# Performance work log

Hardware: AMD Instinct MI355X
Metric: run time of the kernel (lower is better)

The kernel has to match this reference:

```python
import jax, jax.numpy as jnp
import numpy as np

N_USERS = 4096
N_ITEMS = 4096
D = 64
L = 2
B = 4096
N = N_USERS + N_ITEMS


def setup_inputs() -> dict:
    key = jax.random.key(0)
    ks = jax.random.split(key, 24)
    g = lambda i, shape: jax.random.normal(ks[i], shape, dtype=jnp.float32) * 0.05
    # sparse-ish 0/1 adjacency (module calls adj.to_dense(); ~16 neighbors/node)
    adj = (jax.random.uniform(ks[0], (N, N), dtype=jnp.float32) < 0.002).astype(jnp.float32)
    users = jax.random.randint(ks[1], (B,), 0, N_USERS)
    pos_items = jax.random.randint(ks[2], (B,), 0, N_ITEMS)
    neg_items = jax.random.randint(ks[3], (B,), 0, N_ITEMS)
    return {
        "adj_matrix": adj,
        "users": users,
        "pos_items": pos_items,
        "neg_items": neg_items,
        "user_table": g(4, (N_USERS, D)),
        "item_table": g(5, (N_ITEMS, D)),
        "gcn_W": g(6, (L, D, D)), "gcn_b": g(7, (L, D)),
        "gat_W": g(8, (L, D, D)), "gat_b": g(9, (L, D)),
        "attn_W": g(10, (L, 2 * D)), "attn_b": g(11, (L,)),
        "fuse_W": g(12, (L, 2 * D, D)), "fuse_b": g(13, (L, D)),
        "actor_W": g(14, (D, D)), "actor_b": g(15, (D,)),
        "critic_W1": g(16, (2 * D, D)), "critic_b1": g(17, (D,)),
        "critic_W2": g(18, (D, 1)), "critic_b2": g(19, (1,)),
        "layer_weights": jnp.ones((L,), dtype=jnp.float32),
    }


def _leaky(x):
    return jnp.where(x >= 0, x, 0.01 * x)  # F.leaky_relu default slope


def reference(adj_matrix, users, pos_items, neg_items, user_table, item_table,
              gcn_W, gcn_b, gat_W, gat_b, attn_W, attn_b, fuse_W, fuse_b,
              actor_W, actor_b, critic_W1, critic_b1, critic_W2, critic_b2,
              layer_weights):
    all_emb = jnp.concatenate([user_table, item_table], axis=0)  # [N, D]

    # GCN stack: spmm(adj, x) then linear, relu
    gcn = [all_emb]
    for l in range(L):
        h = adj_matrix @ gcn[-1]
        gcn.append(jax.nn.relu(h @ gcn_W[l] + gcn_b[l]))

    # GAT stack: e[i,j] = leaky_relu(a1.h_i + a2.h_j + b); multiply-mask by adj, row softmax
    gat = [all_emb]
    for l in range(L):
        h = gat[-1] @ gat_W[l] + gat_b[l]  # [N, D]
        a1, a2 = attn_W[l, :D], attn_W[l, D:]
        e = _leaky((h @ a1)[:, None] + (h @ a2)[None, :] + attn_b[l])  # [N, N]
        attn = jax.nn.softmax(e * adj_matrix, axis=1)  # faithful: multiply-mask, not -inf
        gat.append(jax.nn.relu(attn @ h))

    lw = jax.nn.softmax(layer_weights)
    fused = jnp.zeros((N, D), dtype=all_emb.dtype)
    for i in range(L):
        cat = jnp.concatenate([gcn[i + 1], gat[i + 1]], axis=1)  # [N, 2D]
        fused = fused + lw[i] * jax.nn.relu(cat @ fuse_W[i] + fuse_b[i])

    user_emb, item_emb = fused[:N_USERS], fused[N_USERS:]
    u = user_emb[users]
    p = item_emb[pos_items]
    n = item_emb[neg_items]

    uf = u @ actor_W + actor_b  # Actor
    pos_score = jnp.sum(uf * p, axis=1)
    neg_score = jnp.sum(uf * n, axis=1)

    def critic(a, b):
        x = jnp.concatenate([a, b], axis=1)
        hidden = jax.nn.relu(x @ critic_W1 + critic_b1)
        return hidden @ critic_W2 + critic_b2

    return pos_score, neg_score, critic(u, p), critic(u, n)
```

## Files before the change

kernel.cpp:

```cpp
#include <hip/hip_runtime.h>

#define NTOT 8192
#define NROW 2048
#define NU 4096
#define D 64
#define MAXN 64
#define ND (NTOT*D)

__device__ __forceinline__ float wsum(float x){
  #pragma unroll
  for(int o=32;o;o>>=1) x += __shfl_xor(x,o);
  return x;
}
__device__ __forceinline__ float wmax(float x){
  #pragma unroll
  for(int o=32;o;o>>=1) x = fmaxf(x,__shfl_xor(x,o));
  return x;
}
__device__ __forceinline__ float bcastf(float x, int k){
  return __uint_as_float(__builtin_amdgcn_readlane(__float_as_uint(x), (unsigned)k));
}
__device__ __forceinline__ int bcasti(int x, int k){
  return (int)__builtin_amdgcn_readlane((unsigned)x, (unsigned)k);
}

__device__ __forceinline__ float gat_attn_row(const float* __restrict__ h,
    const float* __restrict__ kvv, const float* __restrict__ S,
    const int* __restrict__ cols, int cnt, float q, float ab, int lane){
  int t = lane;
  int col = (t < cnt) ? cols[t] : 0;
  float e = -1e30f;
  if(t < cnt){
    float xx = q + kvv[col] + ab;
    e = (xx >= 0.f) ? xx : 0.01f * xx;
  }
  float m  = fmaxf(0.f, wmax(e));
  float w  = (t < cnt) ? expf(e - m) : 0.f;
  float em = expf(-m);
  float Z  = (float)(NTOT - cnt) * em + wsum(w);
  float acc = 0.f, hsum = 0.f;
  for(int tt = 0; tt < cnt; ++tt){
    float wt = bcastf(w, tt);
    int   jc = bcasti(col, tt);
    float hv = h[jc*D + lane];
    acc  = fmaf(wt, hv, acc);
    hsum += hv;
  }
  float outv = (acc + em * (S[lane] - hsum)) / Z;
  return fmaxf(outv, 0.f);
}

__global__ __launch_bounds__(256) void kA(const float* __restrict__ adj,
    const float* __restrict__ ut, const float* __restrict__ it,
    float* __restrict__ all_emb, int* __restrict__ ell, int* __restrict__ nnz,
    float* __restrict__ Svec0, float* __restrict__ Svec1, float* __restrict__ gcn1){
  int bid = blockIdx.x, tid = threadIdx.x;
  if(bid < NROW){
    int lane = tid & 63;
    int row  = bid*4 + (tid >> 6);
    ell[row*MAXN + lane] = NTOT;
    const float4* arow = (const float4*)(adj + (size_t)row * NTOT);
    int base = 0;
    for(int c0 = 0; c0 < NTOT/4; c0 += 64){
      float4 v = arow[c0 + lane];
      int nib = (v.x!=0.f?1:0) | (v.y!=0.f?2:0) | (v.z!=0.f?4:0) | (v.w!=0.f?8:0);
      if(__ballot(nib != 0) == 0ull) continue;
      #pragma unroll
      for(int j = 0; j < 4; ++j){
        unsigned long long m = __ballot(((nib>>j)&1) != 0);
        if(m){
          if((nib>>j)&1){
            int below = __builtin_amdgcn_mbcnt_hi((unsigned)(m>>32),
                        __builtin_amdgcn_mbcnt_lo((unsigned)m, 0u));
            int slot = base + below;
            if(slot < MAXN) ell[row*MAXN + slot] = (c0 + lane)*4 + j;
          }
          base += __popcll(m);
        }
      }
    }
    if(lane == 0) nnz[row] = base > MAXN ? MAXN : base;
  } else if(bid < 2*NROW){
    int i = (bid - NROW)*256 + tid;
    all_emb[i] = (i < NU*D) ? ut[i] : it[i - NU*D];
  } else {
    if(tid < D){
      Svec0[tid] = 0.f; Svec1[tid] = 0.f;
      all_emb[ND + tid] = 0.f;
      gcn1[ND + tid]    = 0.f;
    }
  }
}

__global__ __launch_bounds__(256) void kB(const float* __restrict__ all_emb,
    const int* __restrict__ ell, const int* __restrict__ nnz,
    const float* __restrict__ gcn_W, const float* __restrict__ gcn_b,
    const float* __restrict__ gat_W, const float* __restrict__ gat_b,
    const float* __restrict__ attn_W,
    float* __restrict__ gcn1, float* __restrict__ h0,
    float* __restrict__ qv0, float* __restrict__ kv0, float* __restrict__ Svec0){
  __shared__ float Ws[D*D];
  __shared__ float red[4][D];
  int tid = threadIdx.x, lane = tid & 63, wid = tid >> 6;
  int bid = blockIdx.x;
  if(bid < NROW){
    for(int i = tid; i < D*D; i += 256) Ws[i] = gcn_W[i];
    __syncthreads();
    int row = bid*4 + wid;
    int cnt = nnz[row];
    const int* cols = ell + row*MAXN;
    float acc = 0.f;
    int cnt8 = (cnt + 7) & ~7;
    for(int t = 0; t < cnt8; t += 8){
      #pragma unroll
      for(int u = 0; u < 8; ++u){
        int j = cols[t + u];
        acc += all_emb[j*D + lane];
      }
    }
    float y = gcn_b[lane];
    #pragma unroll 16
    for(int k = 0; k < D; ++k) y = fmaf(bcastf(acc, k), Ws[k*D + lane], y);
    gcn1[row*D + lane] = fmaxf(y, 0.f);
  } else {
    for(int i = tid; i < D*D; i += 256) Ws[i] = gat_W[i];
    __syncthreads();
    int row = (bid - NROW)*4 + wid;
    float xr = all_emb[row*D + lane];
    float h = gat_b[lane];
    #pragma unroll 16
    for(int k = 0; k < D; ++k) h = fmaf(bcastf(xr, k), Ws[k*D + lane], h);
    h0[row*D + lane] = h;
    float q  = wsum(h * attn_W[lane]);
    float kk = wsum(h * attn_W[D + lane]);
    if(lane == 0){ qv0[row] = q; kv0[row] = kk; }
    red[wid][lane] = h;
    __syncthreads();
    if(wid == 0){
      float s = red[0][lane] + red[1][lane] + red[2][lane] + red[3][lane];
      atomicAdd(&Svec0[lane], s);
    }
  }
}

__global__ __launch_bounds__(256) void kC(
    const float* __restrict__ all_emb, const int* __restrict__ ell, const int* __restrict__ nnz,
    const float* __restrict__ gcn1, const float* __restrict__ h0,
    const float* __restrict__ qv0, const float* __restrict__ kv0, const float* __restrict__ Svec0,
    const float* __restrict__ gcn_W, const float* __restrict__ gcn_b,
    const float* __restrict__ gat_W, const float* __restrict__ gat_b,
    const float* __restrict__ attn_W, const float* __restrict__ attn_b,
    const float* __restrict__ fuse_W, const float* __restrict__ fuse_b,
    const float* __restrict__ layer_w,
    float* __restrict__ gcn2, float* __restrict__ h1,
    float* __restrict__ qv1, float* __restrict__ kv1, float* __restrict__ Svec1,
    float* __restrict__ fusedb){
  __shared__ float Ws[D*D];
  __shared__ float red[4][D];
  int tid = threadIdx.x, lane = tid & 63, wid = tid >> 6;
  int bid = blockIdx.x;
  if(bid < NROW){
    for(int i = tid; i < D*D; i += 256) Ws[i] = gcn_W[D*D + i];
    __syncthreads();
    int row = bid*4 + wid;
    int cnt = nnz[row];
    const int* cols = ell + row*MAXN;
    float acc = 0.f;
    int cnt8 = (cnt + 7) & ~7;
    for(int t = 0; t < cnt8; t += 8){
      #pragma unroll
      for(int u = 0; u < 8; ++u){
        int j = cols[t + u];
        acc += gcn1[j*D + lane];
      }
    }
    float y = gcn_b[D + lane];
    #pragma unroll 16
    for(int k = 0; k < D; ++k) y = fmaf(bcastf(acc, k), Ws[k*D + lane], y);
    gcn2[row*D + lane] = fmaxf(y, 0.f);
  } else {
    int row = (bid - NROW)*4 + wid;
    int cnt = nnz[row];
    const int* cols = ell + row*MAXN;
    float g1 = gat_attn_row(h0, kv0, Svec0, cols, cnt, qv0[row], attn_b[0], lane);
    float gc1 = gcn1[row*D + lane];
    float l0 = layer_w[0], l1 = layer_w[1];
    float mx = fmaxf(l0, l1);
    float e0 = expf(l0 - mx), e1 = expf(l1 - mx);
    float lw0 = e0 / (e0 + e1);
    for(int i = tid; i < D*D; i += 256) Ws[i] = fuse_W[i];
    __syncthreads();
    float y = fuse_b[lane];
    #pragma unroll 16
    for(int k = 0; k < D; ++k) y = fmaf(bcastf(gc1, k), Ws[k*D + lane], y);
    __syncthreads();
    for(int i = tid; i < D*D; i += 256) Ws[i] = fuse_W[D*D + i];
    __syncthreads();
    #pragma unroll 16
    for(int k = 0; k < D; ++k) y = fmaf(bcastf(g1, k), Ws[k*D + lane], y);
    fusedb[row*D + lane] = lw0 * fmaxf(y, 0.f);
    __syncthreads();
    for(int i = tid; i < D*D; i += 256) Ws[i] = gat_W[D*D + i];
    __syncthreads();
    float h = gat_b[D + lane];
    #pragma unroll 16
    for(int k = 0; k < D; ++k) h = fmaf(bcastf(g1, k), Ws[k*D + lane], h);
    h1[row*D + lane] = h;
    float qq = wsum(h * attn_W[2*D + lane]);
    float kk = wsum(h * attn_W[3*D + lane]);
    if(lane == 0){ qv1[row] = qq; kv1[row] = kk; }
    red[wid][lane] = h;
    __syncthreads();
    if(wid == 0){
      float s = red[0][lane] + red[1][lane] + red[2][lane] + red[3][lane];
      atomicAdd(&Svec1[lane], s);
    }
  }
}

__global__ __launch_bounds__(256) void kE(
    const int* __restrict__ ell, const int* __restrict__ nnz,
    const float* __restrict__ gcn2, const float* __restrict__ h1,
    const float* __restrict__ qv1, const float* __restrict__ kv1, const float* __restrict__ Svec1,
    const float* __restrict__ attn_b,
    const float* __restrict__ fuse_W, const float* __restrict__ fuse_b,
    const float* __restrict__ layer_w,
    float* __restrict__ fusedb){
  __shared__ float Ws[D*D];
  int tid = threadIdx.x, lane = tid & 63, wid = tid >> 6;
  int row = blockIdx.x*4 + wid;
  int cnt = nnz[row];
  const int* cols = ell + row*MAXN;
  float g2 = gat_attn_row(h1, kv1, Svec1, cols, cnt, qv1[row], attn_b[1], lane);
  float gc2 = gcn2[row*D + lane];
  float l0 = layer_w[0], l1 = layer_w[1];
  float mx = fmaxf(l0, l1);
  float e0 = expf(l0 - mx), e1 = expf(l1 - mx);
  float lw1 = e1 / (e0 + e1);
  for(int i = tid; i < D*D; i += 256) Ws[i] = fuse_W[2*D*D + i];
  __syncthreads();
  float y = fuse_b[D + lane];
  #pragma unroll 16
  for(int k = 0; k < D; ++k) y = fmaf(bcastf(gc2, k), Ws[k*D + lane], y);
  __syncthreads();
  for(int i = tid; i < D*D; i += 256) Ws[i] = fuse_W[3*D*D + i];
  __syncthreads();
  #pragma unroll 16
  for(int k = 0; k < D; ++k) y = fmaf(bcastf(g2, k), Ws[k*D + lane], y);
  fusedb[row*D + lane] += lw1 * fmaxf(y, 0.f);
}

__global__ __launch_bounds__(256) void kF(const float* __restrict__ fused,
    const int* __restrict__ users, const int* __restrict__ pos, const int* __restrict__ neg,
    const float* __restrict__ AW, const float* __restrict__ abias,
    const float* __restrict__ cW1, const float* __restrict__ cb1,
    const float* __restrict__ cW2, const float* __restrict__ cb2,
    float* __restrict__ out){
  __shared__ float AWs[D*D];
  __shared__ float C1s[2*D*D];
  __shared__ float abs_[D], cb1s[D], C2s[D];
  int tid = threadIdx.x;
  for(int i = tid; i < D*D; i += 256) AWs[i] = AW[i];
  for(int i = tid; i < 2*D*D; i += 256) C1s[i] = cW1[i];
  if(tid < D){
    abs_[tid] = abias[tid];
    cb1s[tid] = cb1[tid];
    C2s[tid]  = cW2[tid];
  }
  __syncthreads();
  int lane = tid & 63;
  int bi   = blockIdx.x*4 + (tid >> 6);
  int ui = users[bi], pi = pos[bi] + NU, ni = neg[bi] + NU;
  float ud = fused[ui*D + lane], pd = fused[pi*D + lane], nd = fused[ni*D + lane];
  float ufd = abs_[lane];
  #pragma unroll 16
  for(int k = 0; k < D; ++k) ufd = fmaf(bcastf(ud, k), AWs[k*D + lane], ufd);
  float ps = wsum(ufd * pd);
  float ns = wsum(ufd * nd);
  float hu = cb1s[lane];
  #pragma unroll 16
  for(int k = 0; k < D; ++k) hu = fmaf(bcastf(ud, k), C1s[k*D + lane], hu);
  float hp = hu, hn = hu;
  #pragma unroll 16
  for(int k = 0; k < D; ++k){
    float pk = bcastf(pd, k), nk = bcastf(nd, k);
    hp = fmaf(pk, C1s[(D+k)*D + lane], hp);
    hn = fmaf(nk, C1s[(D+k)*D + lane], hn);
  }
  hp = fmaxf(hp, 0.f); hn = fmaxf(hn, 0.f);
  float cp = wsum(hp * C2s[lane]);
  float cn = wsum(hn * C2s[lane]);
  if(lane == 0){
    out[bi]         = ps;
    out[4096  + bi] = ns;
    out[8192  + bi] = cp + cb2[0];
    out[12288 + bi] = cn + cb2[0];
  }
}

extern "C" void kernel_launch(void* const* d_in, const int* in_sizes, int n_in,
                              void* d_out, int out_size, void* d_ws, size_t ws_size,
                              hipStream_t stream){
  const float* adj        = (const float*)d_in[0];
  const int*   users      = (const int*)d_in[1];
  const int*   pos        = (const int*)d_in[2];
  const int*   neg        = (const int*)d_in[3];
  const float* user_table = (const float*)d_in[4];
  const float* item_table = (const float*)d_in[5];
  const float* gcn_W      = (const float*)d_in[6];
  const float* gcn_b      = (const float*)d_in[7];
  const float* gat_W      = (const float*)d_in[8];
  const float* gat_b      = (const float*)d_in[9];
  const float* attn_W     = (const float*)d_in[10];
  const float* attn_b     = (const float*)d_in[11];
  const float* fuse_W     = (const float*)d_in[12];
  const float* fuse_b     = (const float*)d_in[13];
  const float* actor_W    = (const float*)d_in[14];
  const float* actor_b    = (const float*)d_in[15];
  const float* cW1        = (const float*)d_in[16];
  const float* cb1        = (const float*)d_in[17];
  const float* cW2        = (const float*)d_in[18];
  const float* cb2        = (const float*)d_in[19];
  const float* layer_w    = (const float*)d_in[20];

  float* ws      = (float*)d_ws;
  float* all_emb = ws;
  float* gcn1    = all_emb + ND + D;
  float* gcn2    = gcn1 + ND + D;
  float* h0      = gcn2 + ND;
  float* h1      = h0 + ND;
  float* fusedb  = h1 + ND;
  float* qv0     = fusedb + ND;
  float* kv0     = qv0 + NTOT;
  float* qv1     = kv0 + NTOT;
  float* kv1     = qv1 + NTOT;
  float* Svec0   = kv1 + NTOT;
  float* Svec1   = Svec0 + D;
  int*   nnz     = (int*)(Svec1 + D);
  int*   ell     = nnz + NTOT;

  kA<<<2*NROW + 1, 256, 0, stream>>>(adj, user_table, item_table,
                                     all_emb, ell, nnz, Svec0, Svec1, gcn1);
  kB<<<2*NROW, 256, 0, stream>>>(all_emb, ell, nnz, gcn_W, gcn_b, gat_W, gat_b,
                                 attn_W, gcn1, h0, qv0, kv0, Svec0);
  kC<<<2*NROW, 256, 0, stream>>>(all_emb, ell, nnz, gcn1, h0, qv0, kv0, Svec0,
                                 gcn_W, gcn_b, gat_W, gat_b, attn_W, attn_b,
                                 fuse_W, fuse_b, layer_w,
                                 gcn2, h1, qv1, kv1, Svec1, fusedb);
  kE<<<NROW, 256, 0, stream>>>(ell, nnz, gcn2, h1, qv1, kv1, Svec1, attn_b,
                               fuse_W, fuse_b, layer_w, fusedb);
  kF<<<1024, 256, 0, stream>>>(fusedb, users, pos, neg, actor_W, actor_b,
                               cW1, cb1, cW2, cb2, (float*)d_out);
}
```

Baseline: 221.1 us.

## Fuse adjacency scan with layer-1 GCN/GAT and replace atomics with partial-sum reduction

Restructures the pipeline: the GAT layer-0 projection runs first, then one kernel scans the dense adjacency row into a shared-memory column list and immediately performs GCN and GAT layer-1 aggregation, fusion and the next projection. Layer-2 GCN aggregation moves into the final per-row kernel, so GCN and GAT gathers share one neighbour loop. Atomic column sums are replaced by per-block partials reduced in a small single-block kernel, and adjacency loads are marked nontemporal. This cuts the number of passes and launches over the data, at the cost of two tiny serial reduction launches and heavier per-block work.

```diff
diff --git a/kernel.cpp b/kernel.cpp
--- a/kernel.cpp
+++ b/kernel.cpp
@@ -7,6 +7,8 @@
 #define MAXN 64
 #define ND (NTOT*D)
 
+typedef float f4 __attribute__((ext_vector_type(4)));
+
 __device__ __forceinline__ float wsum(float x){
   #pragma unroll
   for(int o=32;o;o>>=1) x += __shfl_xor(x,o);
@@ -18,210 +20,160 @@
   return x;
 }
 __device__ __forceinline__ float bcastf(float x, int k){
-  return __uint_as_float(__builtin_amdgcn_readlane(__float_as_uint(x), (unsigned)k));
+  return __uint_as_float(__builtin_amdgcn_readlane(__float_as_uint(x),(unsigned)k));
 }
 __device__ __forceinline__ int bcasti(int x, int k){
-  return (int)__builtin_amdgcn_readlane((unsigned)x, (unsigned)k);
-}
-
-__device__ __forceinline__ float gat_attn_row(const float* __restrict__ h,
-    const float* __restrict__ kvv, const float* __restrict__ S,
-    const int* __restrict__ cols, int cnt, float q, float ab, int lane){
-  int t = lane;
-  int col = (t < cnt) ? cols[t] : 0;
-  float e = -1e30f;
-  if(t < cnt){
-    float xx = q + kvv[col] + ab;
-    e = (xx >= 0.f) ? xx : 0.01f * xx;
-  }
-  float m  = fmaxf(0.f, wmax(e));
-  float w  = (t < cnt) ? expf(e - m) : 0.f;
-  float em = expf(-m);
-  float Z  = (float)(NTOT - cnt) * em + wsum(w);
-  float acc = 0.f, hsum = 0.f;
-  for(int tt = 0; tt < cnt; ++tt){
-    float wt = bcastf(w, tt);
-    int   jc = bcasti(col, tt);
-    float hv = h[jc*D + lane];
-    acc  = fmaf(wt, hv, acc);
-    hsum += hv;
-  }
-  float outv = (acc + em * (S[lane] - hsum)) / Z;
-  return fmaxf(outv, 0.f);
-}
-
-__global__ __launch_bounds__(256) void kA(const float* __restrict__ adj,
-    const float* __restrict__ ut, const float* __restrict__ it,
-    float* __restrict__ all_emb, int* __restrict__ ell, int* __restrict__ nnz,
-    float* __restrict__ Svec0, float* __restrict__ Svec1, float* __restrict__ gcn1){
-  int bid = blockIdx.x, tid = threadIdx.x;
-  if(bid < NROW){
-    int lane = tid & 63;
-    int row  = bid*4 + (tid >> 6);
-    ell[row*MAXN + lane] = NTOT;
-    const float4* arow = (const float4*)(adj + (size_t)row * NTOT);
-    int base = 0;
-    for(int c0 = 0; c0 < NTOT/4; c0 += 64){
-      float4 v = arow[c0 + lane];
-      int nib = (v.x!=0.f?1:0) | (v.y!=0.f?2:0) | (v.z!=0.f?4:0) | (v.w!=0.f?8:0);
-      if(__ballot(nib != 0) == 0ull) continue;
-      #pragma unroll
-      for(int j = 0; j < 4; ++j){
-        unsigned long long m = __ballot(((nib>>j)&1) != 0);
-        if(m){
-          if((nib>>j)&1){
-            int below = __builtin_amdgcn_mbcnt_hi((unsigned)(m>>32),
-                        __builtin_amdgcn_mbcnt_lo((unsigned)m, 0u));
-            int slot = base + below;
-            if(slot < MAXN) ell[row*MAXN + slot] = (c0 + lane)*4 + j;
-          }
-          base += __popcll(m);
-        }
-      }
-    }
-    if(lane == 0) nnz[row] = base > MAXN ? MAXN : base;
-  } else if(bid < 2*NROW){
-    int i = (bid - NROW)*256 + tid;
-    all_emb[i] = (i < NU*D) ? ut[i] : it[i - NU*D];
-  } else {
-    if(tid < D){
-      Svec0[tid] = 0.f; Svec1[tid] = 0.f;
-      all_emb[ND + tid] = 0.f;
-      gcn1[ND + tid]    = 0.f;
-    }
-  }
-}
-
-__global__ __launch_bounds__(256) void kB(const float* __restrict__ all_emb,
-    const int* __restrict__ ell, const int* __restrict__ nnz,
-    const float* __restrict__ gcn_W, const float* __restrict__ gcn_b,
-    const float* __restrict__ gat_W, const float* __restrict__ gat_b,
-    const float* __restrict__ attn_W,
-    float* __restrict__ gcn1, float* __restrict__ h0,
-    float* __restrict__ qv0, float* __restrict__ kv0, float* __restrict__ Svec0){
+  return (int)__builtin_amdgcn_readlane((unsigned)x,(unsigned)k);
+}
+
+__global__ __launch_bounds__(256) void k0a(const float* __restrict__ ut, const float* __restrict__ it,
+    const float* __restrict__ gat_W, const float* __restrict__ gat_b, const float* __restrict__ attn_W,
+    float* __restrict__ all_emb, float* __restrict__ h0,
+    float* __restrict__ q0v, float* __restrict__ k0v, float* __restrict__ part0){
   __shared__ float Ws[D*D];
   __shared__ float red[4][D];
   int tid = threadIdx.x, lane = tid & 63, wid = tid >> 6;
-  int bid = blockIdx.x;
-  if(bid < NROW){
-    for(int i = tid; i < D*D; i += 256) Ws[i] = gcn_W[i];
-    __syncthreads();
-    int row = bid*4 + wid;
-    int cnt = nnz[row];
-    const int* cols = ell + row*MAXN;
-    float acc = 0.f;
-    int cnt8 = (cnt + 7) & ~7;
-    for(int t = 0; t < cnt8; t += 8){
-      #pragma unroll
-      for(int u = 0; u < 8; ++u){
-        int j = cols[t + u];
-        acc += all_emb[j*D + lane];
-      }
-    }
-    float y = gcn_b[lane];
-    #pragma unroll 16
-    for(int k = 0; k < D; ++k) y = fmaf(bcastf(acc, k), Ws[k*D + lane], y);
-    gcn1[row*D + lane] = fmaxf(y, 0.f);
-  } else {
-    for(int i = tid; i < D*D; i += 256) Ws[i] = gat_W[i];
-    __syncthreads();
-    int row = (bid - NROW)*4 + wid;
-    float xr = all_emb[row*D + lane];
-    float h = gat_b[lane];
-    #pragma unroll 16
-    for(int k = 0; k < D; ++k) h = fmaf(bcastf(xr, k), Ws[k*D + lane], h);
-    h0[row*D + lane] = h;
-    float q  = wsum(h * attn_W[lane]);
-    float kk = wsum(h * attn_W[D + lane]);
-    if(lane == 0){ qv0[row] = q; kv0[row] = kk; }
-    red[wid][lane] = h;
-    __syncthreads();
-    if(wid == 0){
-      float s = red[0][lane] + red[1][lane] + red[2][lane] + red[3][lane];
-      atomicAdd(&Svec0[lane], s);
-    }
-  }
-}
-
-__global__ __launch_bounds__(256) void kC(
-    const float* __restrict__ all_emb, const int* __restrict__ ell, const int* __restrict__ nnz,
-    const float* __restrict__ gcn1, const float* __restrict__ h0,
-    const float* __restrict__ qv0, const float* __restrict__ kv0, const float* __restrict__ Svec0,
+  for(int i = tid; i < D*D; i += 256) Ws[i] = gat_W[i];
+  __syncthreads();
+  int row = blockIdx.x*4 + wid;
+  float x = (row < NU) ? ut[row*D + lane] : it[(row-NU)*D + lane];
+  all_emb[row*D + lane] = x;
+  float h = gat_b[lane];
+  #pragma unroll 16
+  for(int k = 0; k < D; ++k) h = fmaf(bcastf(x, k), Ws[k*D + lane], h);
+  h0[row*D + lane] = h;
+  float q  = wsum(h * attn_W[lane]);
+  float kk = wsum(h * attn_W[D + lane]);
+  if(lane == 0){ q0v[row] = q; k0v[row] = kk; }
+  red[wid][lane] = h;
+  __syncthreads();
+  if(wid == 0)
+    part0[blockIdx.x*D + lane] = red[0][lane] + red[1][lane] + red[2][lane] + red[3][lane];
+}
+
+__global__ __launch_bounds__(256) void kred(const float* __restrict__ part, float* __restrict__ S){
+  __shared__ float red[4][D];
+  int tid = threadIdx.x, lane = tid & 63, w = tid >> 6;
+  float s = 0.f;
+  for(int i = w; i < NROW; i += 4) s += part[i*D + lane];
+  red[w][lane] = s;
+  __syncthreads();
+  if(tid < D) S[tid] = red[0][tid] + red[1][tid] + red[2][tid] + red[3][tid];
+}
+
+__global__ __launch_bounds__(256) void k1(const float* __restrict__ adj,
+    const float* __restrict__ all_emb, const float* __restrict__ h0,
+    const float* __restrict__ q0v, const float* __restrict__ k0v, const float* __restrict__ S0,
     const float* __restrict__ gcn_W, const float* __restrict__ gcn_b,
     const float* __restrict__ gat_W, const float* __restrict__ gat_b,
     const float* __restrict__ attn_W, const float* __restrict__ attn_b,
     const float* __restrict__ fuse_W, const float* __restrict__ fuse_b,
     const float* __restrict__ layer_w,
-    float* __restrict__ gcn2, float* __restrict__ h1,
-    float* __restrict__ qv1, float* __restrict__ kv1, float* __restrict__ Svec1,
-    float* __restrict__ fusedb){
+    int* __restrict__ ell, int* __restrict__ nnz,
+    float* __restrict__ gcn1, float* __restrict__ fusedb, float* __restrict__ h1,
+    float* __restrict__ q1v, float* __restrict__ k1v, float* __restrict__ part1){
   __shared__ float Ws[D*D];
+  __shared__ int colbuf[4][MAXN];
   __shared__ float red[4][D];
   int tid = threadIdx.x, lane = tid & 63, wid = tid >> 6;
-  int bid = blockIdx.x;
-  if(bid < NROW){
-    for(int i = tid; i < D*D; i += 256) Ws[i] = gcn_W[D*D + i];
-    __syncthreads();
-    int row = bid*4 + wid;
-    int cnt = nnz[row];
-    const int* cols = ell + row*MAXN;
-    float acc = 0.f;
-    int cnt8 = (cnt + 7) & ~7;
-    for(int t = 0; t < cnt8; t += 8){
-      #pragma unroll
-      for(int u = 0; u < 8; ++u){
-        int j = cols[t + u];
-        acc += gcn1[j*D + lane];
+  int row = blockIdx.x*4 + wid;
+
+  const f4* arow = (const f4*)(adj + (size_t)row * NTOT);
+  int base = 0;
+  for(int c0 = 0; c0 < NTOT/4; c0 += 64){
+    f4 v = __builtin_nontemporal_load(&arow[c0 + lane]);
+    int nib = (v.x!=0.f?1:0) | (v.y!=0.f?2:0) | (v.z!=0.f?4:0) | (v.w!=0.f?8:0);
+    if(__ballot(nib != 0) == 0ull) continue;
+    #pragma unroll
+    for(int j = 0; j < 4; ++j){
+      unsigned long long m = __ballot(((nib>>j)&1) != 0);
+      if(m){
+        if((nib>>j)&1){
+          int below = __builtin_amdgcn_mbcnt_hi((unsigned)(m>>32),
+                      __builtin_amdgcn_mbcnt_lo((unsigned)m, 0u));
+          int slot = base + below;
+          if(slot < MAXN) colbuf[wid][slot] = (c0 + lane)*4 + j;
+        }
+        base += __popcll(m);
       }
     }
-    float y = gcn_b[D + lane];
-    #pragma unroll 16
-    for(int k = 0; k < D; ++k) y = fmaf(bcastf(acc, k), Ws[k*D + lane], y);
-    gcn2[row*D + lane] = fmaxf(y, 0.f);
-  } else {
-    int row = (bid - NROW)*4 + wid;
-    int cnt = nnz[row];
-    const int* cols = ell + row*MAXN;
-    float g1 = gat_attn_row(h0, kv0, Svec0, cols, cnt, qv0[row], attn_b[0], lane);
-    float gc1 = gcn1[row*D + lane];
-    float l0 = layer_w[0], l1 = layer_w[1];
-    float mx = fmaxf(l0, l1);
-    float e0 = expf(l0 - mx), e1 = expf(l1 - mx);
-    float lw0 = e0 / (e0 + e1);
-    for(int i = tid; i < D*D; i += 256) Ws[i] = fuse_W[i];
-    __syncthreads();
-    float y = fuse_b[lane];
-    #pragma unroll 16
-    for(int k = 0; k < D; ++k) y = fmaf(bcastf(gc1, k), Ws[k*D + lane], y);
-    __syncthreads();
-    for(int i = tid; i < D*D; i += 256) Ws[i] = fuse_W[D*D + i];
-    __syncthreads();
-    #pragma unroll 16
-    for(int k = 0; k < D; ++k) y = fmaf(bcastf(g1, k), Ws[k*D + lane], y);
-    fusedb[row*D + lane] = lw0 * fmaxf(y, 0.f);
-    __syncthreads();
-    for(int i = tid; i < D*D; i += 256) Ws[i] = gat_W[D*D + i];
-    __syncthreads();
-    float h = gat_b[D + lane];
-    #pragma unroll 16
-    for(int k = 0; k < D; ++k) h = fmaf(bcastf(g1, k), Ws[k*D + lane], h);
-    h1[row*D + lane] = h;
-    float qq = wsum(h * attn_W[2*D + lane]);
-    float kk = wsum(h * attn_W[3*D + lane]);
-    if(lane == 0){ qv1[row] = qq; kv1[row] = kk; }
-    red[wid][lane] = h;
-    __syncthreads();
-    if(wid == 0){
-      float s = red[0][lane] + red[1][lane] + red[2][lane] + red[3][lane];
-      atomicAdd(&Svec1[lane], s);
-    }
-  }
-}
-
-__global__ __launch_bounds__(256) void kE(
+  }
+  int cnt = base > MAXN ? MAXN : base;
+  int mycol = colbuf[wid][lane];
+  if(lane == 0) nnz[row] = cnt;
+  ell[row*MAXN + lane] = mycol;
+
+  float q  = q0v[row];
+  float ab = attn_b[0];
+  int colg = (lane < cnt) ? mycol : 0;
+  float e = -1e30f;
+  if(lane < cnt){
+    float xx = q + k0v[colg] + ab;
+    e = (xx >= 0.f) ? xx : 0.01f * xx;
+  }
+  float m  = fmaxf(0.f, wmax(e));
+  float w  = (lane < cnt) ? expf(e - m) : 0.f;
+  float em = expf(-m);
+  float Z  = (float)(NTOT - cnt) * em + wsum(w);
+
+  float accg = 0.f, acca = 0.f, hs = 0.f;
+  for(int tt = 0; tt < cnt; ++tt){
+    int   c  = bcasti(mycol, tt);
+    float wt = bcastf(w, tt);
+    float ev = all_emb[c*D + lane];
+    float hv = h0[c*D + lane];
+    accg += ev;
+    acca  = fmaf(wt, hv, acca);
+    hs   += hv;
+  }
+  float g1 = fmaxf((acca + em*(S0[lane] - hs)) / Z, 0.f);
+
+  for(int i = tid; i < D*D; i += 256) Ws[i] = gcn_W[i];
+  __syncthreads();
+  float yg = gcn_b[lane];
+  #pragma unroll 16
+  for(int k = 0; k < D; ++k) yg = fmaf(bcastf(accg, k), Ws[k*D + lane], yg);
+  float gc1 = fmaxf(yg, 0.f);
+  gcn1[row*D + lane] = gc1;
+  __syncthreads();
+
+  float l0 = layer_w[0], l1 = layer_w[1];
+  float mx = fmaxf(l0, l1);
+  float e0 = expf(l0 - mx), e1 = expf(l1 - mx);
+  float lw0 = e0 / (e0 + e1);
+  for(int i = tid; i < D*D; i += 256) Ws[i] = fuse_W[i];
+  __syncthreads();
+  float y = fuse_b[lane];
+  #pragma unroll 16
+  for(int k = 0; k < D; ++k) y = fmaf(bcastf(gc1, k), Ws[k*D + lane], y);
+  __syncthreads();
+  for(int i = tid; i < D*D; i += 256) Ws[i] = fuse_W[D*D + i];
+  __syncthreads();
+  #pragma unroll 16
+  for(int k = 0; k < D; ++k) y = fmaf(bcastf(g1, k), Ws[k*D + lane], y);
+  fusedb[row*D + lane] = lw0 * fmaxf(y, 0.f);
+  __syncthreads();
+
+  for(int i = tid; i < D*D; i += 256) Ws[i] = gat_W[D*D + i];
+  __syncthreads();
+  float h = gat_b[D + lane];
+  #pragma unroll 16
+  for(int k = 0; k < D; ++k) h = fmaf(bcastf(g1, k), Ws[k*D + lane], h);
+  h1[row*D + lane] = h;
+  float qq = wsum(h * attn_W[2*D + lane]);
+  float kk = wsum(h * attn_W[3*D + lane]);
+  if(lane == 0){ q1v[row] = qq; k1v[row] = kk; }
+  red[wid][lane] = h;
+  __syncthreads();
+  if(wid == 0)
+    part1[blockIdx.x*D + lane] = red[0][lane] + red[1][lane] + red[2][lane] + red[3][lane];
+}
+
+__global__ __launch_bounds__(256) void k2(
     const int* __restrict__ ell, const int* __restrict__ nnz,
-    const float* __restrict__ gcn2, const float* __restrict__ h1,
-    const float* __restrict__ qv1, const float* __restrict__ kv1, const float* __restrict__ Svec1,
+    const float* __restrict__ gcn1, const float* __restrict__ h1,
+    const float* __restrict__ q1v, const float* __restrict__ k1v, const float* __restrict__ S1,
+    const float* __restrict__ gcn_W, const float* __restrict__ gcn_b,
     const float* __restrict__ attn_b,
     const float* __restrict__ fuse_W, const float* __restrict__ fuse_b,
     const float* __restrict__ layer_w,
@@ -230,9 +182,39 @@
   int tid = threadIdx.x, lane = tid & 63, wid = tid >> 6;
   int row = blockIdx.x*4 + wid;
   int cnt = nnz[row];
-  const int* cols = ell + row*MAXN;
-  float g2 = gat_attn_row(h1, kv1, Svec1, cols, cnt, qv1[row], attn_b[1], lane);
-  float gc2 = gcn2[row*D + lane];
+  int mycol = ell[row*MAXN + lane];
+  float q  = q1v[row];
+  float ab = attn_b[1];
+  int colg = (lane < cnt) ? mycol : 0;
+  float e = -1e30f;
+  if(lane < cnt){
+    float xx = q + k1v[colg] + ab;
+    e = (xx >= 0.f) ? xx : 0.01f * xx;
+  }
+  float m  = fmaxf(0.f, wmax(e));
+  float w  = (lane < cnt) ? expf(e - m) : 0.f;
+  float em = expf(-m);
+  float Z  = (float)(NTOT - cnt) * em + wsum(w);
+  float accg = 0.f, acca = 0.f, hs = 0.f;
+  for(int tt = 0; tt < cnt; ++tt){
+    int   c  = bcasti(mycol, tt);
+    float wt = bcastf(w, tt);
+    float gv = gcn1[c*D + lane];
+    float hv = h1[c*D + lane];
+    accg += gv;
+    acca  = fmaf(wt, hv, acca);
+    hs   += hv;
+  }
+  float g2 = fmaxf((acca + em*(S1[lane] - hs)) / Z, 0.f);
+
+  for(int i = tid; i < D*D; i += 256) Ws[i] = gcn_W[D*D + i];
+  __syncthreads();
+  float yg = gcn_b[D + lane];
+  #pragma unroll 16
+  for(int k = 0; k < D; ++k) yg = fmaf(bcastf(accg, k), Ws[k*D + lane], yg);
+  float gc2 = fmaxf(yg, 0.f);
+  __syncthreads();
+
   float l0 = layer_w[0], l1 = layer_w[1];
   float mx = fmaxf(l0, l1);
   float e0 = expf(l0 - mx), e1 = expf(l1 - mx);
@@ -250,7 +232,7 @@
   fusedb[row*D + lane] += lw1 * fmaxf(y, 0.f);
 }
 
-__global__ __launch_bounds__(256) void kF(const float* __restrict__ fused,
+__global__ __launch_bounds__(256) void k3(const float* __restrict__ fused,
     const int* __restrict__ users, const int* __restrict__ pos, const int* __restrict__ neg,
     const float* __restrict__ AW, const float* __restrict__ abias,
     const float* __restrict__ cW1, const float* __restrict__ cb1,
@@ -325,30 +307,32 @@
 
   float* ws      = (float*)d_ws;
   float* all_emb = ws;
-  float* gcn1    = all_emb + ND + D;
-  float* gcn2    = gcn1 + ND + D;
-  float* h0      = gcn2 + ND;
+  float* h0      = all_emb + ND;
   float* h1      = h0 + ND;
-  float* fusedb  = h1 + ND;
-  float* qv0     = fusedb + ND;
-  float* kv0     = qv0 + NTOT;
-  float* qv1     = kv0 + NTOT;
-  float* kv1     = qv1 + NTOT;
-  float* Svec0   = kv1 + NTOT;
-  float* Svec1   = Svec0 + D;
-  int*   nnz     = (int*)(Svec1 + D);
+  float* gcn1    = h1 + ND;
+  float* fusedb  = gcn1 + ND;
+  float* q0v     = fusedb + ND;
+  float* k0v     = q0v + NTOT;
+  float* q1v     = k0v + NTOT;
+  float* k1v     = q1v + NTOT;
+  float* S0      = k1v + NTOT;
+  float* S1      = S0 + D;
+  float* part0   = S1 + D;
+  float* part1   = part0 + NROW*D;
+  int*   nnz     = (int*)(part1 + NROW*D);
   int*   ell     = nnz + NTOT;
 
-  kA<<<2*NROW + 1, 256, 0, stream>>>(adj, user_table, item_table,
-                                     all_emb, ell, nnz, Svec0, Svec1, gcn1);
-  kB<<<2*NROW, 256, 0, stream>>>(all_emb, ell, nnz, gcn_W, gcn_b, gat_W, gat_b,
-                                 attn_W, gcn1, h0, qv0, kv0, Svec0);
-  kC<<<2*NROW, 256, 0, stream>>>(all_emb, ell, nnz, gcn1, h0, qv0, kv0, Svec0,
-                                 gcn_W, gcn_b, gat_W, gat_b, attn_W, attn_b,
-                                 fuse_W, fuse_b, layer_w,
-                                 gcn2, h1, qv1, kv1, Svec1, fusedb);
-  kE<<<NROW, 256, 0, stream>>>(ell, nnz, gcn2, h1, qv1, kv1, Svec1, attn_b,
-                               fuse_W, fuse_b, layer_w, fusedb);
-  kF<<<1024, 256, 0, stream>>>(fusedb, users, pos, neg, actor_W, actor_b,
+  k0a<<<NROW, 256, 0, stream>>>(user_table, item_table, gat_W, gat_b, attn_W,
+                                all_emb, h0, q0v, k0v, part0);
+  kred<<<1, 256, 0, stream>>>(part0, S0);
+  k1<<<NROW, 256, 0, stream>>>(adj, all_emb, h0, q0v, k0v, S0,
+                               gcn_W, gcn_b, gat_W, gat_b, attn_W, attn_b,
+                               fuse_W, fuse_b, layer_w,
+                               ell, nnz, gcn1, fusedb, h1, q1v, k1v, part1);
+  kred<<<1, 256, 0, stream>>>(part1, S1);
+  k2<<<NROW, 256, 0, stream>>>(ell, nnz, gcn1, h1, q1v, k1v, S1,
+                               gcn_W, gcn_b, attn_b, fuse_W, fuse_b, layer_w,
+                               fusedb);
+  k3<<<1024, 256, 0, stream>>>(fusedb, users, pos, neg, actor_W, actor_b,
                                cW1, cb1, cW2, cb2, (float*)d_out);
 }
```

Result: slower. 368.4 us (+66.6%).
